# Performance work log

Measured on AMD Instinct MI355X. Metric: run time of the kernel, lower is better.

## Reference

```python
import jax, jax.numpy as jnp
import numpy as np

N = 100_000
E = 1_600_000
D_IN, D_HID, D_OUT = 512, 256, 256


def setup_inputs() -> dict:
    key = jax.random.key(0)
    ks = jax.random.split(key, 10)
    x = jax.random.normal(ks[0], (N, D_IN), dtype=jnp.float32)
    edge_index = jax.random.randint(ks[1], (2, E), 0, N, dtype=jnp.int64)
    edge_weight = jax.random.uniform(ks[2], (E,), dtype=jnp.float32)
    # Glorot-ish init for the per-layer linear weights (PyG GCNConv: Linear w/o bias, bias added after aggregation)
    W1 = jax.random.normal(ks[3], (D_IN, D_HID), dtype=jnp.float32) * (1.0 / np.sqrt(D_IN))
    b1 = jnp.zeros((D_HID,), dtype=jnp.float32)
    W2 = jax.random.normal(ks[4], (D_HID, D_HID), dtype=jnp.float32) * (1.0 / np.sqrt(D_HID))
    b2 = jnp.zeros((D_HID,), dtype=jnp.float32)
    W3 = jax.random.normal(ks[5], (D_HID, D_OUT), dtype=jnp.float32) * (1.0 / np.sqrt(D_HID))
    b3 = jnp.zeros((D_OUT,), dtype=jnp.float32)
    return {"x": x, "edge_index": edge_index, "edge_weight": edge_weight,
            "W1": W1, "b1": b1, "W2": W2, "b2": b2, "W3": W3, "b3": b3}


def gcn_layer(h_in, W, b, row, col, ew, n):
    # PyG GCNConv with normalize=True, add_self_loops=True (fill value 1.0), aggr='add':
    # h = X W; deg[i] = sum of incoming edge weights (incl. self loop);
    # norm_e = deg^-1/2[row] * w_e * deg^-1/2[col]; out[col] += norm_e * h[row]; out += bias
    h = h_in @ W                                            # [n, d_out]
    deg = jnp.zeros((n,), h.dtype).at[col].add(ew) + 1.0    # +1 from self loop
    dinv = jnp.where(deg > 0, jax.lax.rsqrt(deg), 0.0)      # deg_inv_sqrt, inf -> 0
    norm = dinv[row] * ew * dinv[col]                       # [E]
    out = jnp.zeros_like(h).at[col].add(norm[:, None] * h[row])
    out = out + (dinv * dinv)[:, None] * h                  # self-loop contribution (norm_ii = dinv_i^2)
    return out + b


def reference(x, edge_index, edge_weight, W1, b1, W2, b2, W3, b3):
    row, col = edge_index[0], edge_index[1]
    n = x.shape[0]
    # dropout p=0.0 -> identity
    h = jax.nn.relu(gcn_layer(x, W1, b1, row, col, edge_weight, n))
    h = jax.nn.relu(gcn_layer(h, W2, b2, row, col, edge_weight, n))
    return gcn_layer(h, W3, b3, row, col, edge_weight, n)
```

## Files before the change

### kernel.cpp

```cpp
#include <hip/hip_runtime.h>
#include <hip/hip_bf16.h>


#define D 256
#define ELLW 48

typedef unsigned short ushort_t;
typedef unsigned long long u64;
typedef float f32x4 __attribute__((ext_vector_type(4)));
typedef short bf16x8 __attribute__((ext_vector_type(8)));
typedef unsigned int u32x4 __attribute__((ext_vector_type(4)));

__device__ __forceinline__ float blo(unsigned u) { return __uint_as_float(u << 16); }
__device__ __forceinline__ float bhi(unsigned u) { return __uint_as_float(u & 0xFFFF0000u); }
__device__ __forceinline__ ushort_t f2b(float f) {
    unsigned u = __float_as_uint(f);
    return (ushort_t)((u + 0x7FFFu + ((u >> 16) & 1u)) >> 16);
}
__device__ __forceinline__ void gload_lds16(const ushort_t* g, ushort_t* l) {
    __builtin_amdgcn_global_load_lds((const __attribute__((address_space(1))) unsigned int*)g,
                                     (__attribute__((address_space(3))) unsigned int*)l, 16, 0, 0);
}

__global__ __launch_bounds__(256) void scatter_ell(const int* __restrict__ row,
                                                   const int* __restrict__ col,
                                                   const float* __restrict__ ew,
                                                   int* __restrict__ cnt,
                                                   u64* __restrict__ ell, int E) {
    int e = blockIdx.x * 256 + threadIdx.x;
    if (e < E) {
        int c = __builtin_nontemporal_load(&col[e]);
        int r = __builtin_nontemporal_load(&row[e]);
        float w = __builtin_nontemporal_load(&ew[e]);
        int pos = atomicAdd(&cnt[c], 1);
        if (pos < ELLW) {
            u64 rec = ((u64)__float_as_uint(w) << 32) | (unsigned)r;
            __builtin_nontemporal_store(rec, &ell[(size_t)c * ELLW + pos]);
        }
    }
}

__global__ __launch_bounds__(256) void dinv_ell(const int* __restrict__ cnt,
                                                const u64* __restrict__ ell,
                                                float* __restrict__ dinv, int N) {
    int node = blockIdx.x * 4 + (threadIdx.x >> 6);
    if (node >= N) return;
    int lane = threadIdx.x & 63;
    int m = cnt[node];
    if (m > ELLW) m = ELLW;
    float w = 0.f;
    if (lane < m) w = __uint_as_float((unsigned)(ell[(size_t)node * ELLW + lane] >> 32));
#pragma unroll
    for (int off = 32; off > 0; off >>= 1) w += __shfl_xor(w, off);
    if (lane == 0) dinv[node] = rsqrtf(w + 1.0f);
}

__global__ __launch_bounds__(256) void cvtT_kernel(const float* __restrict__ W,
                                                   ushort_t* __restrict__ WT, int K, int C) {
    int i = blockIdx.x * 256 + threadIdx.x;
    if (i < K * C) {
        int c = i / K, k = i - c * K;
        WT[i] = f2b(W[(size_t)k * C + c]);
    }
}

template <int K, bool AF32>
__global__ __launch_bounds__(256) void gemm_mfma(const void* __restrict__ Ap,
                                                 const ushort_t* __restrict__ WT,
                                                 ushort_t* __restrict__ C, int nvalid) {
    __shared__ ushort_t As[128 * 64];
    __shared__ ushort_t Bs[256 * 64];
    const int tid = threadIdx.x;
    const int lane = tid & 63, wave = tid >> 6;
    const int wrow = wave >> 1, wcol = wave & 1;
    const int fr = lane & 15, fq = lane >> 4;
    const int r0 = blockIdx.x * 128;

    f32x4 acc[4][8] = {};

    for (int k0 = 0; k0 < K; k0 += 64) {
        if constexpr (AF32) {
            const float* Af = (const float*)Ap;
#pragma unroll
            for (int i = 0; i < 8; ++i) {
                int idx = i * 256 + tid;
                int rowt = idx >> 4;
                int c4 = idx & 15;
                int grow = r0 + rowt;
                if (grow >= nvalid) grow = nvalid - 1;
                f32x4 v = __builtin_nontemporal_load(
                    (const f32x4*)&Af[(size_t)grow * K + k0 + c4 * 4]);
                ushort4 h;
                h.x = f2b(v[0]); h.y = f2b(v[1]); h.z = f2b(v[2]); h.w = f2b(v[3]);
                int slot = c4 >> 1, half = c4 & 1;
                int off = rowt * 64 + ((slot ^ (rowt & 7)) << 3) + (half << 2);
                *(ushort4*)&As[off] = h;
            }
        } else {
            const ushort_t* Ab = (const ushort_t*)Ap;
#pragma unroll
            for (int q = 0; q < 4; ++q) {
                int qa = wave * 4 + q;
                int rowt = qa * 8 + (lane >> 3);
                int g = (lane & 7) ^ (lane >> 3);
                gload_lds16(&Ab[(size_t)(r0 + rowt) * K + k0 + g * 8], &As[qa * 512]);
            }
        }
#pragma unroll
        for (int q = 0; q < 8; ++q) {
            int qb = wave * 8 + q;
            int rowt = qb * 8 + (lane >> 3);
            int g = (lane & 7) ^ (lane >> 3);
            gload_lds16(&WT[(size_t)rowt * K + k0 + g * 8], &Bs[qb * 512]);
        }
        __syncthreads();

#pragma unroll
        for (int kk = 0; kk < 2; ++kk) {
            int g = (kk * 4 + fq) ^ (fr & 7);
            bf16x8 aF[4];
#pragma unroll
            for (int m = 0; m < 4; ++m) {
                int arow = wrow * 64 + m * 16 + fr;
                aF[m] = *(const bf16x8*)&As[arow * 64 + g * 8];
            }
#pragma unroll
            for (int n = 0; n < 8; ++n) {
                int bcol = wcol * 128 + n * 16 + fr;
                bf16x8 bF = *(const bf16x8*)&Bs[bcol * 64 + g * 8];
#pragma unroll
                for (int m = 0; m < 4; ++m)
                    acc[m][n] = __builtin_amdgcn_mfma_f32_16x16x32_bf16(
                        aF[m], bF, acc[m][n], 0, 0, 0);
            }
        }
        __syncthreads();
    }

#pragma unroll
    for (int m = 0; m < 4; ++m) {
        int gr0 = r0 + wrow * 64 + m * 16 + fq * 4;
#pragma unroll
        for (int n = 0; n < 8; ++n) {
            int gc = wcol * 128 + n * 16 + fr;
#pragma unroll
            for (int r = 0; r < 4; ++r) {
                int gr = gr0 + r;
                if (gr < nvalid) C[(size_t)gr * D + gc] = f2b(acc[m][n][r]);
            }
        }
    }
}

template <bool RELU, bool OUTF32>
__global__ __launch_bounds__(256) void agg_kernel(const ushort_t* __restrict__ hb,
                                                  const float* __restrict__ dinv,
                                                  const float* __restrict__ bias,
                                                  const int* __restrict__ cnt,
                                                  const u64* __restrict__ ell,
                                                  void* __restrict__ outp, int N) {
    int node = blockIdx.x * 4 + (threadIdx.x >> 6);
    if (node >= N) return;
    int lane = threadIdx.x & 63;
    int half = lane >> 5;
    int fl = lane & 31;
    float dn = dinv[node], d2 = dn * dn;

    u32x4 sv = *(const u32x4*)&hb[(size_t)node * 256 + fl * 8];
    float sc = half ? 0.f : d2;
    float a0 = sc * blo(sv.x), a1 = sc * bhi(sv.x);
    float a2 = sc * blo(sv.y), a3 = sc * bhi(sv.y);
    float a4 = sc * blo(sv.z), a5 = sc * bhi(sv.z);
    float a6 = sc * blo(sv.w), a7 = sc * bhi(sv.w);

    int m = cnt[node];
    if (m > ELLW) m = ELLW;
    int srcl = 0;
    float wl = 0.f;
    if (lane < m) {
        u64 r = __builtin_nontemporal_load(&ell[(size_t)node * ELLW + lane]);
        srcl = (int)(unsigned)r;
        wl = dinv[srcl] * __uint_as_float((unsigned)(r >> 32)) * dn;
    }
    int steps = (m + 1) >> 1;
#pragma unroll 4
    for (int j = 0; j < steps; ++j) {
        int idx2 = 2 * j + half;
        int src = __shfl(srcl, idx2);
        float w = __shfl(wl, idx2);
        u32x4 v = *(const u32x4*)&hb[(size_t)src * 256 + fl * 8];
        a0 = fmaf(w, blo(v.x), a0); a1 = fmaf(w, bhi(v.x), a1);
        a2 = fmaf(w, blo(v.y), a2); a3 = fmaf(w, bhi(v.y), a3);
        a4 = fmaf(w, blo(v.z), a4); a5 = fmaf(w, bhi(v.z), a5);
        a6 = fmaf(w, blo(v.w), a6); a7 = fmaf(w, bhi(v.w), a7);
    }
    a0 += __shfl_xor(a0, 32); a1 += __shfl_xor(a1, 32);
    a2 += __shfl_xor(a2, 32); a3 += __shfl_xor(a3, 32);
    a4 += __shfl_xor(a4, 32); a5 += __shfl_xor(a5, 32);
    a6 += __shfl_xor(a6, 32); a7 += __shfl_xor(a7, 32);
    float r0 = half ? a4 : a0;
    float r1 = half ? a5 : a1;
    float r2 = half ? a6 : a2;
    float r3 = half ? a7 : a3;
    f32x4 bb = *(const f32x4*)&bias[fl * 8 + half * 4];
    r0 += bb[0]; r1 += bb[1]; r2 += bb[2]; r3 += bb[3];
    if (RELU) {
        r0 = fmaxf(r0, 0.f); r1 = fmaxf(r1, 0.f);
        r2 = fmaxf(r2, 0.f); r3 = fmaxf(r3, 0.f);
    }
    if (OUTF32) {
        f32x4 o = {r0, r1, r2, r3};
        __builtin_nontemporal_store(
            o, (f32x4*)((float*)outp + (size_t)node * 256 + fl * 8 + half * 4));
    } else {
        u64 p = (u64)f2b(r0) | ((u64)f2b(r1) << 16) | ((u64)f2b(r2) << 32) | ((u64)f2b(r3) << 48);
        __builtin_nontemporal_store(
            p, (u64*)((ushort_t*)outp + (size_t)node * 256 + fl * 8 + half * 4));
    }
}

extern "C" void kernel_launch(void* const* d_in, const int* in_sizes, int n_in,
                              void* d_out, int out_size, void* d_ws, size_t ws_size,
                              hipStream_t stream) {
    const float* x  = (const float*)d_in[0];
    const int*   ei = (const int*)d_in[1];
    const float* ew = (const float*)d_in[2];
    const float* W1 = (const float*)d_in[3];
    const float* b1 = (const float*)d_in[4];
    const float* W2 = (const float*)d_in[5];
    const float* b2 = (const float*)d_in[6];
    const float* W3 = (const float*)d_in[7];
    const float* b3 = (const float*)d_in[8];
    const int N = in_sizes[0] / 512;
    const int E = in_sizes[2];
    const int* row = ei;
    const int* col = ei + E;
    float* out = (float*)d_out;

    const int MB = (N + 127) / 128;
    const size_t Npad = (size_t)MB * 128;

    char* ws = (char*)d_ws;
    size_t off = 0;
    auto alloc = [&](size_t bytes) -> void* {
        void* p = ws + off;
        off += (bytes + 255) / 256 * 256;
        return p;
    };
    ushort_t* hb  = (ushort_t*)alloc(Npad * D * sizeof(ushort_t));
    u64*      ell = (u64*)alloc((size_t)N * ELLW * sizeof(u64));
    ushort_t* WT1 = (ushort_t*)alloc((size_t)512 * D * sizeof(ushort_t));
    ushort_t* WT2 = (ushort_t*)alloc((size_t)256 * D * sizeof(ushort_t));
    ushort_t* WT3 = (ushort_t*)alloc((size_t)256 * D * sizeof(ushort_t));
    int*   cnt    = (int*)alloc((size_t)N * sizeof(int));
    float* dinv   = (float*)alloc((size_t)N * sizeof(float));
    ushort_t* ab  = (ushort_t*)d_out;

    hipMemsetAsync(cnt, 0, (size_t)N * sizeof(int), stream);

    int gE = (E + 255) / 256;
    int gA = (N + 3) / 4;
    cvtT_kernel<<<(512 * D + 255) / 256, 256, 0, stream>>>(W1, WT1, 512, D);
    cvtT_kernel<<<(256 * D + 255) / 256, 256, 0, stream>>>(W2, WT2, 256, D);
    cvtT_kernel<<<(256 * D + 255) / 256, 256, 0, stream>>>(W3, WT3, 256, D);
    scatter_ell<<<gE, 256, 0, stream>>>(row, col, ew, cnt, ell, E);
    dinv_ell<<<gA, 256, 0, stream>>>(cnt, ell, dinv, N);

    gemm_mfma<512, true><<<MB, 256, 0, stream>>>(x, WT1, hb, N);
    agg_kernel<true, false><<<gA, 256, 0, stream>>>(hb, dinv, b1, cnt, ell, ab, N);
    gemm_mfma<256, false><<<MB, 256, 0, stream>>>(ab, WT2, hb, N);
    agg_kernel<true, false><<<gA, 256, 0, stream>>>(hb, dinv, b2, cnt, ell, ab, N);
    gemm_mfma<256, false><<<MB, 256, 0, stream>>>(ab, WT3, hb, N);
    agg_kernel<false, true><<<gA, 256, 0, stream>>>(hb, dinv, b3, cnt, ell, out, N);
}
```

Before: 735.1 us.

## Build ELL graph via two-pass bucketed binning with LDS atomics

Replaces the per-edge global atomic scatter into a per-node ELL layout with a two-pass scheme. Edges are first binned into 128-node buckets with one padded global counter per bucket, then each bucket is processed by one block using LDS atomics to place edges and accumulate degrees. Degree and dinv computation are fused into the second pass, and the bins reuse the hb buffer. This adds a second pass over the edges, and any bucket whose fill exceeds CAP silently drops edges.

```diff
diff --git a/kernel.cpp b/kernel.cpp
--- a/kernel.cpp
+++ b/kernel.cpp
@@ -4,12 +4,15 @@
 
 #define D 256
 #define ELLW 48
+#define BSH 7
+#define CAP 2432
 
 typedef unsigned short ushort_t;
 typedef unsigned long long u64;
 typedef float f32x4 __attribute__((ext_vector_type(4)));
 typedef short bf16x8 __attribute__((ext_vector_type(8)));
 typedef unsigned int u32x4 __attribute__((ext_vector_type(4)));
+typedef int i32x4 __attribute__((ext_vector_type(4)));
 
 __device__ __forceinline__ float blo(unsigned u) { return __uint_as_float(u << 16); }
 __device__ __forceinline__ float bhi(unsigned u) { return __uint_as_float(u & 0xFFFF0000u); }
@@ -22,37 +25,56 @@
                                      (__attribute__((address_space(3))) unsigned int*)l, 16, 0, 0);
 }
 
-__global__ __launch_bounds__(256) void scatter_ell(const int* __restrict__ row,
-                                                   const int* __restrict__ col,
-                                                   const float* __restrict__ ew,
-                                                   int* __restrict__ cnt,
-                                                   u64* __restrict__ ell, int E) {
+__global__ __launch_bounds__(256) void bin_p1(const int* __restrict__ row,
+                                              const int* __restrict__ col,
+                                              const float* __restrict__ ew,
+                                              int* __restrict__ bfill,
+                                              i32x4* __restrict__ bins, int E) {
     int e = blockIdx.x * 256 + threadIdx.x;
     if (e < E) {
         int c = __builtin_nontemporal_load(&col[e]);
         int r = __builtin_nontemporal_load(&row[e]);
         float w = __builtin_nontemporal_load(&ew[e]);
-        int pos = atomicAdd(&cnt[c], 1);
-        if (pos < ELLW) {
-            u64 rec = ((u64)__float_as_uint(w) << 32) | (unsigned)r;
-            __builtin_nontemporal_store(rec, &ell[(size_t)c * ELLW + pos]);
-        }
-    }
-}
-
-__global__ __launch_bounds__(256) void dinv_ell(const int* __restrict__ cnt,
-                                                const u64* __restrict__ ell,
-                                                float* __restrict__ dinv, int N) {
-    int node = blockIdx.x * 4 + (threadIdx.x >> 6);
-    if (node >= N) return;
-    int lane = threadIdx.x & 63;
-    int m = cnt[node];
-    if (m > ELLW) m = ELLW;
-    float w = 0.f;
-    if (lane < m) w = __uint_as_float((unsigned)(ell[(size_t)node * ELLW + lane] >> 32));
-#pragma unroll
-    for (int off = 32; off > 0; off >>= 1) w += __shfl_xor(w, off);
-    if (lane == 0) dinv[node] = rsqrtf(w + 1.0f);
+        int b = c >> BSH;
+        int pos = atomicAdd(&bfill[b * 16], 1);
+        if (pos < CAP) {
+            i32x4 rec = {r, __float_as_int(w), c, 0};
+            __builtin_nontemporal_store(rec, &bins[(size_t)b * CAP + pos]);
+        }
+    }
+}
+
+__global__ __launch_bounds__(256) void bin_p2(const i32x4* __restrict__ bins,
+                                              const int* __restrict__ bfill,
+                                              int* __restrict__ cnt,
+                                              float* __restrict__ dinv,
+                                              u64* __restrict__ ell, int N) {
+    __shared__ int scnt[1 << BSH];
+    __shared__ float ssum[1 << BSH];
+    const int b = blockIdx.x;
+    const int base = b << BSH;
+    const int t = threadIdx.x;
+    if (t < (1 << BSH)) { scnt[t] = 0; ssum[t] = 0.f; }
+    __syncthreads();
+    int fill = bfill[b * 16];
+    if (fill > CAP) fill = CAP;
+    for (int i = t; i < fill; i += 256) {
+        i32x4 rec = bins[(size_t)b * CAP + i];
+        int li = rec.z - base;
+        int pos = atomicAdd(&scnt[li], 1);
+        if (pos < ELLW)
+            ell[(size_t)rec.z * ELLW + pos] = ((u64)(unsigned)rec.y << 32) | (unsigned)rec.x;
+        atomicAdd(&ssum[li], __int_as_float(rec.y));
+    }
+    __syncthreads();
+    if (t < (1 << BSH)) {
+        int node = base + t;
+        if (node < N) {
+            int m = scnt[t];
+            cnt[node] = (m > ELLW) ? ELLW : m;
+            dinv[node] = rsqrtf(ssum[t] + 1.0f);
+        }
+    }
 }
 
 __global__ __launch_bounds__(256) void cvtT_kernel(const float* __restrict__ W,
@@ -174,7 +196,6 @@
     float a6 = sc * blo(sv.w), a7 = sc * bhi(sv.w);
 
     int m = cnt[node];
-    if (m > ELLW) m = ELLW;
     int srcl = 0;
     float wl = 0.f;
     if (lane < m) {
@@ -239,6 +260,7 @@
 
     const int MB = (N + 127) / 128;
     const size_t Npad = (size_t)MB * 128;
+    const int NBU = (N + (1 << BSH) - 1) >> BSH;
 
     char* ws = (char*)d_ws;
     size_t off = 0;
@@ -254,17 +276,19 @@
     ushort_t* WT3 = (ushort_t*)alloc((size_t)256 * D * sizeof(ushort_t));
     int*   cnt    = (int*)alloc((size_t)N * sizeof(int));
     float* dinv   = (float*)alloc((size_t)N * sizeof(float));
+    int*   bfill  = (int*)alloc((size_t)NBU * 16 * sizeof(int));
+    i32x4* bins   = (i32x4*)hb;
     ushort_t* ab  = (ushort_t*)d_out;
 
-    hipMemsetAsync(cnt, 0, (size_t)N * sizeof(int), stream);
+    (void)hipMemsetAsync(bfill, 0, (size_t)NBU * 16 * sizeof(int), stream);
 
     int gE = (E + 255) / 256;
     int gA = (N + 3) / 4;
     cvtT_kernel<<<(512 * D + 255) / 256, 256, 0, stream>>>(W1, WT1, 512, D);
     cvtT_kernel<<<(256 * D + 255) / 256, 256, 0, stream>>>(W2, WT2, 256, D);
     cvtT_kernel<<<(256 * D + 255) / 256, 256, 0, stream>>>(W3, WT3, 256, D);
-    scatter_ell<<<gE, 256, 0, stream>>>(row, col, ew, cnt, ell, E);
-    dinv_ell<<<gA, 256, 0, stream>>>(cnt, ell, dinv, N);
+    bin_p1<<<gE, 256, 0, stream>>>(row, col, ew, bfill, bins, E);
+    bin_p2<<<NBU, 256, 0, stream>>>(bins, bfill, cnt, dinv, ell, N);
 
     gemm_mfma<512, true><<<MB, 256, 0, stream>>>(x, WT1, hb, N);
     agg_kernel<true, false><<<gA, 256, 0, stream>>>(hb, dinv, b1, cnt, ell, ab, N);
```

Result: no change. 727.6 us (-1.0%).
